# Kernel optimization log

Hardware: AMD Instinct MI355X
Metric: run time of the kernel (lower is better)

## Reference

```python
import jax, jax.numpy as jnp
import numpy as np

NX, NY = 128, 128
NT = 50
DECAY = 0.1
M1 = M2 = 12
WIDTH = 64


def _spectral(x, w1, w2):
    # x: [B, W, NX, NY]; w1/w2: complex [W, W, M1, M2]
    xf = jnp.fft.rfft2(x)                                   # [B, W, NX, NY//2+1]
    of = jnp.zeros(xf.shape[:2] + (NX, NY // 2 + 1), jnp.complex64)
    of = of.at[:, :, :M1, :M2].set(jnp.einsum('bixy,ioxy->boxy', xf[:, :, :M1, :M2], w1))
    of = of.at[:, :, NX - M1:, :M2].set(jnp.einsum('bixy,ioxy->boxy', xf[:, :, NX - M1:, :M2], w2))
    return jnp.fft.irfft2(of, s=(NX, NY))


def _forward(xyt_q, obs_coords, obs_vals, x_grid, y_grid,
             fc0_w, fc0_b, spec_w1r, spec_w1i, spec_w2r, spec_w2i,
             pw_w, pw_b, fc1_w, fc1_b, fc2_w, fc2_b,
             nb_idx, sensor_iy, sensor_ix, Lx, Ly):
    B, K = nb_idx.shape
    # ---- gather obs, temporal-decay weight, scatter-add into sparse grid ----
    sensor_ids = nb_idx // NT                               # [B, K]
    t_nb = obs_coords[nb_idx, 2]                            # [B, K]
    w = jnp.exp(-DECAY * jnp.abs(t_nb - xyt_q[:, None, 2])) # [B, K]
    vals = obs_vals[nb_idx] * w                             # [B, K]
    lin = sensor_iy[sensor_ids] * NY + sensor_ix[sensor_ids]
    flat = (lin + jnp.arange(B)[:, None] * (NX * NY)).ravel()
    sparse = jnp.zeros(B * NX * NY, obs_vals.dtype).at[flat].add(vals.ravel())
    counts = jnp.zeros(B * NX * NY, obs_vals.dtype).at[flat].add(w.ravel())
    grid = jnp.where(counts > 0, sparse / jnp.maximum(counts, 1e-6), 0.0).reshape(B, NX, NY)
    # ---- FNO core ----
    inp = jnp.stack([grid,
                     jnp.broadcast_to(x_grid, (B, NX, NY)),
                     jnp.broadcast_to(y_grid, (B, NX, NY))], axis=1)  # [B, 3, NX, NY]
    x = jnp.einsum('bcxy,cw->bwxy', inp, fc0_w) + fc0_b[None, :, None, None]
    for i in range(4):
        y = (_spectral(x, spec_w1r[i] + 1j * spec_w1i[i], spec_w2r[i] + 1j * spec_w2i[i])
             + jnp.einsum('bcxy,oc->boxy', x, pw_w[i]) + pw_b[i][None, :, None, None])
        x = jax.nn.gelu(y, approximate=False) if i < 3 else y
    h = jax.nn.gelu(jnp.einsum('bwxy,wf->bxyf', x, fc1_w) + fc1_b, approximate=False)
    field = (jnp.einsum('bxyf,fo->bxyo', h, fc2_w) + fc2_b).transpose(0, 3, 1, 2)  # [B, 3, NX, NY]
    # ---- bilinear sample at query points ----
    x01 = jnp.clip(xyt_q[:, 0] / max(Lx, 1e-6), 0.0, 1.0)
    y01 = jnp.clip(xyt_q[:, 1] / max(Ly, 1e-6), 0.0, 1.0)
    gx = x01 * (NX - 1)
    gy = y01 * (NY - 1)
    x0 = jnp.floor(gx).astype(jnp.int32)
    y0 = jnp.floor(gy).astype(jnp.int32)
    x1 = jnp.minimum(x0 + 1, NX - 1)
    y1 = jnp.minimum(y0 + 1, NY - 1)
    wx = (gx - x0)[:, None]
    wy = (gy - y0)[:, None]
    b = jnp.arange(B)
    f00 = field[b, :, x0, y0]
    f10 = field[b, :, x1, y0]
    f01 = field[b, :, x0, y1]
    f11 = field[b, :, x1, y1]
    top = f00 * (1.0 - wx) + f10 * wx
    bot = f01 * (1.0 - wx) + f11 * wx
    return top * (1.0 - wy) + bot * wy                       # [B, 3]


def setup_inputs() -> dict:
    key = jax.random.key(0)
    ks = jax.random.split(key, 20)
    B, K, NOBS, NS = 64, 64, 50000, 1000
    scale = 1.0 / (WIDTH * WIDTH)
    inp = {
        'xyt_q': jax.random.uniform(ks[0], (B, 3), jnp.float32),
        'obs_coords': jax.random.uniform(ks[1], (NOBS, 3), jnp.float32),
        'obs_vals': jax.random.normal(ks[2], (NOBS,), jnp.float32),
        'x_grid': jax.random.uniform(ks[3], (NX, NY), jnp.float32),
        'y_grid': jax.random.uniform(ks[4], (NX, NY), jnp.float32),
        'fc0_w': jax.random.normal(ks[5], (3, WIDTH), jnp.float32) * 0.3,
        'fc0_b': jnp.zeros((WIDTH,), jnp.float32),
        'spec_w1r': scale * jax.random.uniform(ks[6], (4, WIDTH, WIDTH, M1, M2), jnp.float32),
        'spec_w1i': scale * jax.random.uniform(ks[7], (4, WIDTH, WIDTH, M1, M2), jnp.float32),
        'spec_w2r': scale * jax.random.uniform(ks[8], (4, WIDTH, WIDTH, M1, M2), jnp.float32),
        'spec_w2i': scale * jax.random.uniform(ks[9], (4, WIDTH, WIDTH, M1, M2), jnp.float32),
        'pw_w': jax.random.normal(ks[10], (4, WIDTH, WIDTH), jnp.float32) * (1.0 / np.sqrt(WIDTH)),
        'pw_b': jnp.zeros((4, WIDTH), jnp.float32),
        'fc1_w': jax.random.normal(ks[11], (WIDTH, 128), jnp.float32) * (1.0 / np.sqrt(WIDTH)),
        'fc1_b': jnp.zeros((128,), jnp.float32),
        'fc2_w': jax.random.normal(ks[12], (128, 3), jnp.float32) * (1.0 / np.sqrt(128.0)),
        'fc2_b': jnp.zeros((3,), jnp.float32),
        'nb_idx': jax.random.randint(ks[13], (B, K), 0, NOBS, jnp.int32),
        'sensor_iy': jax.random.randint(ks[14], (NS,), 0, NX, jnp.int32),
        'sensor_ix': jax.random.randint(ks[15], (NS,), 0, NY, jnp.int32),
        'Lx': 1,
        'Ly': 1,
    }
    return inp


def reference(xyt_q, obs_coords, obs_vals, x_grid, y_grid,
              fc0_w, fc0_b, spec_w1r, spec_w1i, spec_w2r, spec_w2i,
              pw_w, pw_b, fc1_w, fc1_b, fc2_w, fc2_b,
              nb_idx, sensor_iy, sensor_ix, Lx, Ly):
    return _forward(xyt_q, obs_coords, obs_vals, x_grid, y_grid,
                    fc0_w, fc0_b, spec_w1r, spec_w1i, spec_w2r, spec_w2i,
                    pw_w, pw_b, fc1_w, fc1_b, fc2_w, fc2_b,
                    nb_idx, sensor_iy, sensor_ix, Lx, Ly)
```

## Files before the change

kernel.cpp:

```cpp
#include <hip/hip_runtime.h>
#include <math.h>

#define NXg 128
#define NYg 128
#define Pg  (NXg*NYg)
#define Bq  64
#define Wd  64
#define NKX 24
#define NMODE (NKX*12)
#define PI2_128 0.04908738521234052f

typedef _Float16 f16x8 __attribute__((ext_vector_type(8)));
typedef _Float16 f16x4 __attribute__((ext_vector_type(4)));
typedef float    f32x4 __attribute__((ext_vector_type(4)));

#define OFF_TC  0
#define OFF_TS  (OFF_TC + 128)
#define F32_END (OFF_TS + 128)
#define H_T1E  0
#define H_T1ET (H_T1E + 32*128)
#define H_A2   (H_T1ET + 128*32)
#define H_PWH  (H_A2 + 48*256)
#define H_T2ET (H_PWH + 4*64*64)
#define H_XFHR (H_T2ET + 128*64)
#define H_XFHI (H_XFHR + 288*4096)
#define H_OFHR (H_XFHI + 288*4096)
#define H_OFHI (H_OFHR + 288*4096)
#define H_WHR  (H_OFHI + 288*4096)
#define H_WHI  (H_WHR + (size_t)4*288*4096)
#define H_YG   (H_WHI + (size_t)4*288*4096)
#define H_X    (H_YG + (size_t)Bq*Wd*128*24)
#define H_U    (H_X + (size_t)Bq*128*128*64)

__device__ __forceinline__ float fast_gelu(float v) {
    float a = fabsf(v) * 0.70710678118654752f;
    float t = 1.f / (1.f + 0.3275911f * a);
    float p = t * (0.254829592f + t * (-0.284496736f + t * (1.421413741f +
              t * (-1.453152027f + t * 1.061405429f))));
    float er = 1.f - p * __expf(-a * a);
    er = copysignf(er, v);
    return 0.5f * v * (1.f + er);
}

__global__ void k_prep(_Float16* T1e_g, _Float16* T1eT_g, _Float16* A2_g,
                       const float* pww, _Float16* PWh, _Float16* T2eT_g,
                       float* Tc, float* Ts,
                       const float* xyt, const float* obs_c, const float* obs_v,
                       const int* nb, const int* siy, const int* six,
                       float* val, float* cnt,
                       const float* w1r, const float* w1i,
                       const float* w2r, const float* w2i,
                       _Float16* Whr, _Float16* Whi) {
    __shared__ _Float16 L[64][146];
    int blk = blockIdx.x;
    if (blk < 64) {
        int t = blk * 256 + threadIdx.x;
        if (t < 32*128) {
            int r = t >> 7, y = t & 127;
            float v = 0.f;
            if (r < 12)      v =  cosf((float)((r * y) & 127) * PI2_128);
            else if (r < 24) v = -sinf((float)(((r-12) * y) & 127) * PI2_128);
            T1e_g[t] = (_Float16)v;
            int y2 = t >> 5, r2 = t & 31;
            float v2 = 0.f;
            if (r2 < 12)      v2 =  cosf((float)((r2 * y2) & 127) * PI2_128);
            else if (r2 < 24) v2 = -sinf((float)(((r2-12) * y2) & 127) * PI2_128);
            T1eT_g[t] = (_Float16)v2;
        }
        if (t < 48*256) {
            int m = t >> 8, k = t & 255;
            int x = k & 127;
            int hi = (k >= 128);
            float v;
            if (m < 24) {
                int kx = (m < 12) ? m : (104 + m);
                float th = (float)((kx * x) & 127) * PI2_128;
                v = hi ? sinf(th) : cosf(th);
            } else {
                int mm = m - 24;
                int kx = (mm < 12) ? mm : (104 + mm);
                float th = (float)((kx * x) & 127) * PI2_128;
                v = hi ? cosf(th) : -sinf(th);
            }
            A2_g[t] = (_Float16)v;
        }
        if (t < 4*64*64) PWh[t] = (_Float16)pww[t];
        if (t < 128*64) {
            int x = t >> 6, k = t & 63;
            float v = 0.f;
            if (k < 24) {
                int kx = (k < 12) ? k : (104 + k);
                v = cosf((float)((kx * x) & 127) * PI2_128);
            } else if (k < 48) {
                int kk = k - 24;
                int kx = (kk < 12) ? kk : (104 + kk);
                v = sinf((float)((kx * x) & 127) * PI2_128);
            }
            T2eT_g[t] = (_Float16)v;
        }
        if (t < 128) {
            float th = (float)t * PI2_128;
            Tc[t] = cosf(th);
            Ts[t] = sinf(th);
        }
    } else if (blk < 80) {
        int t = (blk - 64) * 256 + threadIdx.x;
        int b = t >> 6;
        int id = nb[t];
        int sid = id / 50;
        float tq = xyt[b*3 + 2];
        float w = expf(-0.1f * fabsf(obs_c[id*3 + 2] - tq));
        int lin = siy[sid] * NYg + six[sid];
        atomicAdd(&val[b*Pg + lin], obs_v[id] * w);
        atomicAdd(&cnt[b*Pg + lin], w);
    } else {
        int u = blk - 80;
        int layer = u >> 8;
        int rem = u & 255;
        int o = rem & 63, ri = (rem >> 6) & 1, half = rem >> 7;
        const float* src = half ? (ri ? w2i : w2r) : (ri ? w1i : w1r);
        _Float16* dst = ri ? Whi : Whr;
        size_t sbase = (size_t)layer * 589824 + (size_t)o * 144;
        for (int idx = threadIdx.x; idx < 9216; idx += 256) {
            int i = idx / 144, m = idx - i*144;
            L[i][m] = (_Float16)src[sbase + (size_t)i*9216 + m];
        }
        __syncthreads();
        size_t obase = ((size_t)(layer*288 + half*144) << 12) + o*64;
        for (int idx = threadIdx.x; idx < 9216; idx += 256) {
            int m = idx >> 6, i = idx & 63;
            dst[obase + ((size_t)m << 12) + i] = L[i][m];
        }
    }
}

__device__ __forceinline__ void stageA_bf(const _Float16* __restrict__ T1e_g, int lane, f16x8* bf) {
    int l15 = lane & 15, quad = lane >> 4;
    #pragma unroll
    for (int u = 0; u < 8; u++) {
        int nt2 = u >> 2, q = u & 3;
        bf[u] = *(const f16x8*)&T1e_g[(nt2*16 + l15)*128 + q*32 + quad*8];
    }
}

__device__ __forceinline__ void stageA_core(const _Float16 (*Xn)[76], const f16x8* bf,
                                            _Float16* __restrict__ Yg, int b, int row, int tid) {
    int wave = tid >> 6, lane = tid & 63;
    int l15 = lane & 15, quad = lane >> 4;
    f16x8 af[4];
    #pragma unroll
    for (int q = 0; q < 4; q++)
        #pragma unroll
        for (int j = 0; j < 8; j++)
            af[q][j] = Xn[q*32 + quad*8 + j][wave*16 + l15];
    #pragma unroll
    for (int nt2 = 0; nt2 < 2; nt2++) {
        f32x4 acc = {0.f,0.f,0.f,0.f};
        #pragma unroll
        for (int q = 0; q < 4; q++)
            acc = __builtin_amdgcn_mfma_f32_16x16x32_f16(af[q], bf[nt2*4 + q], acc, 0, 0, 0);
        int t = nt2*16 + l15;
        if (t < 24) {
            #pragma unroll
            for (int r = 0; r < 4; r++) {
                int o = wave*16 + quad*4 + r;
                Yg[((size_t)(b*64 + o)*128 + row)*24 + t] = (_Float16)acc[r];
            }
        }
    }
}

__device__ __forceinline__ void stageA(const _Float16 (*Xn)[76], const _Float16* __restrict__ T1e_g,
                                       _Float16* __restrict__ Yg, int b, int row, int tid) {
    f16x8 bf[8];
    stageA_bf(T1e_g, tid & 63, bf);
    stageA_core(Xn, bf, Yg, b, row, tid);
}

__global__ __launch_bounds__(256) void k_fc0y(const float* __restrict__ val, const float* __restrict__ cnt,
                      const float* __restrict__ xg, const float* __restrict__ yg,
                      const float* __restrict__ w, const float* __restrict__ bb,
                      const _Float16* __restrict__ T1e_g,
                      _Float16* __restrict__ Yg) {
    __shared__ _Float16 Xn[128][76];
    __shared__ float wl[4][64];
    int row = blockIdx.x, b = blockIdx.y;
    int tid = threadIdx.x;
    if (tid < 64) {
        wl[0][tid] = w[tid]; wl[1][tid] = w[64+tid]; wl[2][tid] = w[128+tid]; wl[3][tid] = bb[tid];
    }
    __syncthreads();
    {
        int y = tid & 127, half = tid >> 7;
        int p = row*128 + y;
        float c = cnt[(size_t)b*Pg + p];
        float g = (c > 0.f) ? val[(size_t)b*Pg + p] / fmaxf(c, 1e-6f) : 0.f;
        float a1 = xg[p], a2 = yg[p];
        #pragma unroll
        for (int blk = 0; blk < 4; blk++) {
            f16x8 pk;
            #pragma unroll
            for (int j = 0; j < 8; j++) {
                int o = half*32 + blk*8 + j;
                pk[j] = (_Float16)(g*wl[0][o] + a1*wl[1][o] + a2*wl[2][o] + wl[3][o]);
            }
            *(f16x8*)&Xn[y][half*32 + blk*8] = pk;
        }
    }
    __syncthreads();
    stageA(Xn, T1e_g, Yg, b, row, tid);
}

__global__ __launch_bounds__(256) void k_sB(const _Float16* __restrict__ Yg,
                    const _Float16* __restrict__ A2_g,
                    _Float16* __restrict__ xfhr, _Float16* __restrict__ xfhi) {
    __shared__ _Float16 Ys[4][28][136];
    int bc4 = blockIdx.x << 2;
    int tid = threadIdx.x;
    int wave = tid >> 6, lane = tid & 63;
    int l15 = lane & 15, quad = lane >> 4;
    const _Float16* base = Yg + (size_t)bc4 * 3072;
    for (int i = tid; i < 1536; i += 256) {
        int s = i / 384, ii = i - s*384;
        f16x8 v = *(const f16x8*)&base[s*3072 + ii*8];
        int e = ii*8;
        #pragma unroll
        for (int j = 0; j < 8; j++) {
            int idx = e + j;
            int x = idx / 24, t = idx - x*24;
            Ys[s][t][x] = v[j];
        }
    }
    __syncthreads();
    int bc = bc4 + wave;
    #pragma unroll
    for (int mt = 0; mt < 3; mt++) {
        f32x4 acc = {0.f,0.f,0.f,0.f};
        #pragma unroll
        for (int q = 0; q < 8; q++) {
            f16x8 a = *(const f16x8*)&A2_g[(size_t)(mt*16 + l15)*256 + q*32 + quad*8];
            const _Float16* brow = (q < 4) ? &Ys[wave][l15][q*32 + quad*8]
                                           : &Ys[wave][12 + l15][(q-4)*32 + quad*8];
            f16x8 bfr = *(const f16x8*)brow;
            acc = __builtin_amdgcn_mfma_f32_16x16x32_f16(a, bfr, acc, 0, 0, 0);
        }
        if (l15 < 12) {
            #pragma unroll
            for (int r = 0; r < 4; r++) {
                int m = mt*16 + quad*4 + r;
                if (m < 24) xfhr[(size_t)(m*12 + l15)*4096 + bc] = (_Float16)acc[r];
                else        xfhi[(size_t)((m-24)*12 + l15)*4096 + bc] = (_Float16)acc[r];
            }
        }
    }
}

__global__ __launch_bounds__(256) void k_s3m(const _Float16* __restrict__ xfhr, const _Float16* __restrict__ xfhi,
                    const _Float16* __restrict__ Whr, const _Float16* __restrict__ Whi,
                    _Float16* __restrict__ ofhr, _Float16* __restrict__ ofhi, int layer) {
    __shared__ _Float16 Xr[16][72], Xi[16][72];
    int mode = blockIdx.x;
    int bo = blockIdx.y << 4;
    int tid = threadIdx.x;
    int wave = tid >> 6, lane = tid & 63;
    int l15 = lane & 15, quad = lane >> 4;
    const _Float16* pr = xfhr + (size_t)mode * 4096 + bo*64;
    const _Float16* pi = xfhi + (size_t)mode * 4096 + bo*64;
    if (tid < 128) {
        int b = tid >> 3, seg = tid & 7;
        *(f16x8*)&Xr[b][seg*8] = *(const f16x8*)&pr[tid*8];
        *(f16x8*)&Xi[b][seg*8] = *(const f16x8*)&pi[tid*8];
    }
    __syncthreads();
    size_t wb = ((size_t)(layer*288 + mode)*64 + wave*16 + l15) * 64 + quad*8;
    f16x8 wr0 = *(const f16x8*)&Whr[wb];
    f16x8 wr1 = *(const f16x8*)&Whr[wb + 32];
    f16x8 wi0 = *(const f16x8*)&Whi[wb];
    f16x8 wi1 = *(const f16x8*)&Whi[wb + 32];
    f16x8 xr0 = *(const f16x8*)&Xr[l15][quad*8];
    f16x8 xr1 = *(const f16x8*)&Xr[l15][32 + quad*8];
    f16x8 xi0 = *(const f16x8*)&Xi[l15][quad*8];
    f16x8 xi1 = *(const f16x8*)&Xi[l15][32 + quad*8];
    f16x8 xn0, xn1;
    #pragma unroll
    for (int j = 0; j < 8; j++) { xn0[j] = -xi0[j]; xn1[j] = -xi1[j]; }
    f32x4 cr = {0.f,0.f,0.f,0.f}, ci = {0.f,0.f,0.f,0.f};
    cr = __builtin_amdgcn_mfma_f32_16x16x32_f16(xr0, wr0, cr, 0, 0, 0);
    cr = __builtin_amdgcn_mfma_f32_16x16x32_f16(xr1, wr1, cr, 0, 0, 0);
    cr = __builtin_amdgcn_mfma_f32_16x16x32_f16(xn0, wi0, cr, 0, 0, 0);
    cr = __builtin_amdgcn_mfma_f32_16x16x32_f16(xn1, wi1, cr, 0, 0, 0);
    ci = __builtin_amdgcn_mfma_f32_16x16x32_f16(xr0, wi0, ci, 0, 0, 0);
    ci = __builtin_amdgcn_mfma_f32_16x16x32_f16(xr1, wi1, ci, 0, 0, 0);
    ci = __builtin_amdgcn_mfma_f32_16x16x32_f16(xi0, wr0, ci, 0, 0, 0);
    ci = __builtin_amdgcn_mfma_f32_16x16x32_f16(xi1, wr1, ci, 0, 0, 0);
    #pragma unroll
    for (int r = 0; r < 4; r++) {
        int b = bo + quad*4 + r;
        int o = wave*16 + l15;
        ofhr[(size_t)mode*4096 + b*64 + o] = (_Float16)cr[r];
        ofhi[(size_t)mode*4096 + b*64 + o] = (_Float16)ci[r];
    }
}

__global__ __launch_bounds__(256) void k_sG(const _Float16* __restrict__ ofhr, const _Float16* __restrict__ ofhi,
                    const _Float16* __restrict__ T2eT_g, _Float16* __restrict__ Gh) {
    __shared__ _Float16 As[64][72];
    __shared__ _Float16 Cs[128][72];
    int b = blockIdx.x, t = blockIdx.y;
    int tid = threadIdx.x;
    int wave = tid >> 6, lane = tid & 63;
    int l15 = lane & 15, quad = lane >> 4;
    int ky = (t < 12) ? t : (t - 12);
    float sc = ((ky == 0) ? 1.f : 2.f) * (1.f/16384.f);
    bool isReal = (t < 12);
    if (tid < 192) {
        int kxi = tid >> 3, seg = tid & 7;
        size_t idx = (size_t)(kxi*12 + ky)*4096 + b*64 + seg*8;
        f16x8 vr8 = *(const f16x8*)&ofhr[idx];
        f16x8 vi8 = *(const f16x8*)&ofhi[idx];
        #pragma unroll
        for (int j = 0; j < 8; j++) {
            int o = seg*8 + j;
            float vr = (float)vr8[j] * sc, vi = (float)vi8[j] * sc;
            As[o][kxi]      = (_Float16)(isReal ? vr : vi);
            As[o][24 + kxi] = (_Float16)(isReal ? -vi : vr);
        }
    }
    for (int i = tid; i < 1024; i += 256)
        As[i >> 4][48 + (i & 15)] = (_Float16)0.f;
    __syncthreads();
    f16x8 a0 = *(const f16x8*)&As[wave*16 + l15][quad*8];
    f16x8 a1 = *(const f16x8*)&As[wave*16 + l15][32 + quad*8];
    #pragma unroll
    for (int nt = 0; nt < 8; nt++) {
        f16x8 b0 = *(const f16x8*)&T2eT_g[(nt*16 + l15)*64 + quad*8];
        f16x8 b1 = *(const f16x8*)&T2eT_g[(nt*16 + l15)*64 + 32 + quad*8];
        f32x4 acc = {0.f,0.f,0.f,0.f};
        acc = __builtin_amdgcn_mfma_f32_16x16x32_f16(a0, b0, acc, 0, 0, 0);
        acc = __builtin_amdgcn_mfma_f32_16x16x32_f16(a1, b1, acc, 0, 0, 0);
        f16x4 pk;
        #pragma unroll
        for (int r = 0; r < 4; r++) pk[r] = (_Float16)acc[r];
        *(f16x4*)&Cs[nt*16 + l15][wave*16 + quad*4] = pk;
    }
    __syncthreads();
    float4* o4 = (float4*)Gh;
    for (int i = tid; i < 1024; i += 256) {
        int x = i >> 3, seg = i & 7;
        o4[((size_t)((b*128 + x)*24 + t))*8 + seg] = *(const float4*)&Cs[x][seg*8];
    }
}

__global__ __launch_bounds__(256, 4) void k_s45(_Float16* __restrict__ xh,
                    const _Float16* __restrict__ Gh,
                    const _Float16* __restrict__ T1e_g, const _Float16* __restrict__ T1eT_g,
                    const _Float16* __restrict__ PWh,
                    const float* __restrict__ pwb,
                    _Float16* __restrict__ Yg, int layer,
                    const float* __restrict__ xyt, const int* __restrict__ Lx,
                    const float* __restrict__ val, const float* __restrict__ cnt,
                    const float* __restrict__ xg, const float* __restrict__ yg,
                    const float* __restrict__ fc0w, const float* __restrict__ fc0b) {
    __shared__ _Float16 BsT[2][128][76];
    __shared__ float wl[4][64];
    int rp = blockIdx.x, b = blockIdx.y;
    int row0 = rp << 1;
    int tid = threadIdx.x;
    int wave = tid >> 6, lane = tid & 63;
    int l15 = lane & 15, quad = lane >> 4;

    f16x8 af2[2];
    #pragma unroll
    for (int r2 = 0; r2 < 2; r2++)
        #pragma unroll
        for (int j = 0; j < 8; j++) af2[r2][j] = (_Float16)0.f;
    if (quad < 3) {
        #pragma unroll
        for (int r2 = 0; r2 < 2; r2++) {
            const _Float16* gt = Gh + (size_t)(b*128 + row0 + r2) * 1536 + wave*16 + l15;
            #pragma unroll
            for (int j = 0; j < 8; j++) af2[r2][j] = gt[(quad*8 + j) * 64];
        }
    }

    f16x8 af0 = *(const f16x8*)&PWh[(size_t)(layer*64 + wave*16 + l15)*64 + quad*8];
    f16x8 af1 = *(const f16x8*)&PWh[(size_t)(layer*64 + wave*16 + l15)*64 + 32 + quad*8];
    f16x8 b2a[8];
    #pragma unroll
    for (int nt = 0; nt < 8; nt++)
        b2a[nt] = *(const f16x8*)&T1eT_g[(nt*16 + l15)*32 + quad*8];
    float pb[4];
    #pragma unroll
    for (int r = 0; r < 4; r++)
        pb[r] = pwb[layer*64 + wave*16 + quad*4 + r];

    if (layer == 0) {
        if (tid < 64) {
            wl[0][tid] = fc0w[tid]; wl[1][tid] = fc0w[64+tid];
            wl[2][tid] = fc0w[128+tid]; wl[3][tid] = fc0b[tid];
        }
        __syncthreads();
        int y = tid & 127, half = tid >> 7;
        #pragma unroll
        for (int r2 = 0; r2 < 2; r2++) {
            int p = (row0 + r2)*128 + y;
            float c = cnt[(size_t)b*Pg + p];
            float g = (c > 0.f) ? val[(size_t)b*Pg + p] / fmaxf(c, 1e-6f) : 0.f;
            float a1 = xg[p], a2 = yg[p];
            #pragma unroll
            for (int blk = 0; blk < 4; blk++) {
                f16x8 pkk;
                #pragma unroll
                for (int j = 0; j < 8; j++) {
                    int o = half*32 + blk*8 + j;
                    pkk[j] = (_Float16)(g*wl[0][o] + a1*wl[1][o] + a2*wl[2][o] + wl[3][o]);
                }
                *(f16x8*)&BsT[r2][y][half*32 + blk*8] = pkk;
            }
        }
    } else {
        for (int i = tid; i < 2048; i += 256) {
            int r2 = i >> 10, k = i & 1023;
            int y = k >> 3, seg = k & 7;
            *(float4*)&BsT[r2][y][seg*8] =
                ((const float4*)(xh + (size_t)(b*128 + row0 + r2) * 8192))[k];
        }
    }
    __syncthreads();

    f16x4 pk[2][8];
    #pragma unroll
    for (int r2 = 0; r2 < 2; r2++) {
        f32x4 acc[8];
        #pragma unroll
        for (int nt = 0; nt < 8; nt++) {
            f32x4 a = {0.f,0.f,0.f,0.f};
            f16x8 b0 = *(const f16x8*)&BsT[r2][nt*16 + l15][quad*8];
            f16x8 b1 = *(const f16x8*)&BsT[r2][nt*16 + l15][32 + quad*8];
            a = __builtin_amdgcn_mfma_f32_16x16x32_f16(af0, b0, a, 0, 0, 0);
            a = __builtin_amdgcn_mfma_f32_16x16x32_f16(af1, b1, a, 0, 0, 0);
            a = __builtin_amdgcn_mfma_f32_16x16x32_f16(af2[r2], b2a[nt], a, 0, 0, 0);
            acc[nt] = a;
        }
        #pragma unroll
        for (int nt = 0; nt < 8; nt++)
            #pragma unroll
            for (int r = 0; r < 4; r++)
                pk[r2][nt][r] = (_Float16)fast_gelu(acc[nt][r] + pb[r]);
    }
    __syncthreads();

    #pragma unroll
    for (int r2 = 0; r2 < 2; r2++)
        #pragma unroll
        for (int nt = 0; nt < 8; nt++)
            *(f16x4*)&BsT[r2][nt*16 + l15][wave*16 + quad*4] = pk[r2][nt];
    __syncthreads();

    bool st0 = true, st1 = true;
    if (layer == 2) {
        float Lxf = fmaxf((float)Lx[0], 1e-6f);
        float x01 = fminf(fmaxf(xyt[b*3 + 0] / Lxf, 0.f), 1.f);
        float gxp = x01 * (NXg - 1);
        int x0 = (int)floorf(gxp);
        int x1 = min(x0 + 1, NXg - 1);
        st0 = (row0 == x0) || (row0 == x1);
        st1 = (row0 + 1 == x0) || (row0 + 1 == x1);
    }
    for (int i = tid; i < 2048; i += 256) {
        int r2 = i >> 10, k = i & 1023;
        if (r2 ? st1 : st0) {
            int y = k >> 3, seg = k & 7;
            ((float4*)(xh + (size_t)(b*128 + row0 + r2) * 8192))[k] =
                *(const float4*)&BsT[r2][y][seg*8];
        }
    }

    f16x8 bf[8];
    stageA_bf(T1e_g, lane, bf);
    stageA_core(BsT[0], bf, Yg, b, row0, tid);
    stageA_core(BsT[1], bf, Yg, b, row0 + 1, tid);
}

__global__ __launch_bounds__(256) void k_final(const _Float16* __restrict__ x,
                    const _Float16* __restrict__ ofhr, const _Float16* __restrict__ ofhi,
                    const float* __restrict__ pw, const float* __restrict__ pwb,
                    const float* __restrict__ fc1w, const float* __restrict__ fc1b,
                    const float* __restrict__ fc2w, const float* __restrict__ fc2b,
                    const float* __restrict__ xyt, const int* __restrict__ Lx, const int* __restrict__ Ly,
                    const float* __restrict__ Tc, const float* __restrict__ Ts,
                    float* __restrict__ out) {
    __shared__ float y4[4][64];
    __shared__ float hh[4][129];
    __shared__ int   pxy[4][2];
    __shared__ float wxy[2];
    __shared__ float tc[128], ts[128];
    int b = blockIdx.x;
    if (threadIdx.x < 128) {
        tc[threadIdx.x] = Tc[threadIdx.x];
        ts[threadIdx.x] = Ts[threadIdx.x];
    }
    if (threadIdx.x == 0) {
        float Lxf = fmaxf((float)Lx[0], 1e-6f);
        float Lyf = fmaxf((float)Ly[0], 1e-6f);
        float x01 = fminf(fmaxf(xyt[b*3 + 0] / Lxf, 0.f), 1.f);
        float y01 = fminf(fmaxf(xyt[b*3 + 1] / Lyf, 0.f), 1.f);
        float gx = x01 * (NXg - 1), gy = y01 * (NYg - 1);
        int x0 = (int)floorf(gx), y0 = (int)floorf(gy);
        int x1 = min(x0 + 1, NXg - 1), y1 = min(y0 + 1, NYg - 1);
        wxy[0] = gx - (float)x0;
        wxy[1] = gy - (float)y0;
        pxy[0][0] = x0; pxy[0][1] = y0;
        pxy[1][0] = x1; pxy[1][1] = y0;
        pxy[2][0] = x0; pxy[2][1] = y1;
        pxy[3][0] = x1; pxy[3][1] = y1;
    }
    __syncthreads();
    {
        int p = threadIdx.x >> 6, o = threadIdx.x & 63;
        int px = pxy[p][0], py = pxy[p][1];
        float gkr[12], gki[12];
        #pragma unroll
        for (int ky = 0; ky < 12; ky++) { gkr[ky] = 0.f; gki[ky] = 0.f; }
        for (int kxi = 0; kxi < 24; kxi++) {
            int kx = (kxi < 12) ? kxi : (104 + kxi);
            int m = (kx * px) & 127;
            float cc = tc[m], ss = ts[m];
            #pragma unroll
            for (int ky = 0; ky < 12; ky++) {
                size_t idx = (size_t)(kxi*12 + ky)*4096 + b*64 + o;
                float a = (float)ofhr[idx], bb = (float)ofhi[idx];
                gkr[ky] += a*cc - bb*ss;
                gki[ky] += a*ss + bb*cc;
            }
        }
        float sp = gkr[0];
        #pragma unroll
        for (int ky = 1; ky < 12; ky++) {
            int m = (ky * py) & 127;
            sp += 2.f * (gkr[ky]*tc[m] - gki[ky]*ts[m]);
        }
        float s = 0.f;
        const _Float16* xb = x + ((size_t)(b*128 + px)*128 + py)*64;
        #pragma unroll 4
        for (int c = 0; c < 64; c++)
            s += pw[3*4096 + o*64 + c] * (float)xb[c];
        y4[p][o] = sp * (1.f/16384.f) + s + pwb[3*64 + o];
    }
    __syncthreads();
    for (int i = threadIdx.x; i < 512; i += 256) {
        int p = i >> 7, f = i & 127;
        float s = fc1b[f];
        #pragma unroll 4
        for (int w = 0; w < 64; w++) s += y4[p][w] * fc1w[w*128 + f];
        hh[p][f] = 0.5f * s * (1.f + erff(s * 0.70710678118654752f));
    }
    __syncthreads();
    if (threadIdx.x < 3) {
        int o3 = threadIdx.x;
        float f4[4];
        #pragma unroll
        for (int p = 0; p < 4; p++) {
            float s = fc2b[o3];
            #pragma unroll 4
            for (int f = 0; f < 128; f++) s += hh[p][f] * fc2w[f*3 + o3];
            f4[p] = s;
        }
        float wx = wxy[0], wy = wxy[1];
        float top = f4[0]*(1.f - wx) + f4[1]*wx;
        float bot = f4[2]*(1.f - wx) + f4[3]*wx;
        out[b*3 + o3] = top*(1.f - wy) + bot*wy;
    }
}

extern "C" void kernel_launch(void* const* d_in, const int* in_sizes, int n_in,
                              void* d_out, int out_size, void* d_ws, size_t ws_size,
                              hipStream_t stream) {
    const float* xyt    = (const float*)d_in[0];
    const float* obs_c  = (const float*)d_in[1];
    const float* obs_v  = (const float*)d_in[2];
    const float* xg     = (const float*)d_in[3];
    const float* yg     = (const float*)d_in[4];
    const float* fc0w   = (const float*)d_in[5];
    const float* fc0b   = (const float*)d_in[6];
    const float* w1r    = (const float*)d_in[7];
    const float* w1i    = (const float*)d_in[8];
    const float* w2r    = (const float*)d_in[9];
    const float* w2i    = (const float*)d_in[10];
    const float* pww    = (const float*)d_in[11];
    const float* pwb    = (const float*)d_in[12];
    const float* fc1w   = (const float*)d_in[13];
    const float* fc1b   = (const float*)d_in[14];
    const float* fc2w   = (const float*)d_in[15];
    const float* fc2b   = (const float*)d_in[16];
    const int*   nb     = (const int*)d_in[17];
    const int*   siy    = (const int*)d_in[18];
    const int*   six    = (const int*)d_in[19];
    const int*   Lx     = (const int*)d_in[20];
    const int*   Ly     = (const int*)d_in[21];
    float* out = (float*)d_out;

    float* W = (float*)d_ws;
    float* Tc  = W + OFF_TC;
    float* Ts  = W + OFF_TS;
    _Float16* Hbase = (_Float16*)(W + F32_END);
    _Float16* T1e_g  = Hbase + H_T1E;
    _Float16* T1eT_g = Hbase + H_T1ET;
    _Float16* A2_g   = Hbase + H_A2;
    _Float16* PWh    = Hbase + H_PWH;
    _Float16* T2eT_g = Hbase + H_T2ET;
    _Float16* xfhr   = Hbase + H_XFHR;
    _Float16* xfhi   = Hbase + H_XFHI;
    _Float16* ofhr   = Hbase + H_OFHR;
    _Float16* ofhi   = Hbase + H_OFHI;
    _Float16* Whr    = Hbase + H_WHR;
    _Float16* Whi    = Hbase + H_WHI;
    _Float16* Yg     = Hbase + H_YG;
    _Float16* xh     = Hbase + H_X;
    float*    val    = (float*)(Hbase + H_U);
    float*    cnt    = val + Bq*Pg;
    _Float16* Gh2    = Hbase + H_U + (size_t)4*Bq*Pg;

    hipMemsetAsync(val, 0, (size_t)2 * Bq * Pg * sizeof(float), stream);

    k_prep<<<1104, 256, 0, stream>>>(T1e_g, T1eT_g, A2_g, pww, PWh, T2eT_g, Tc, Ts,
                                     xyt, obs_c, obs_v, nb, siy, six, val, cnt,
                                     w1r, w1i, w2r, w2i, Whr, Whi);
    k_fc0y<<<dim3(128, Bq), 256, 0, stream>>>(val, cnt, xg, yg, fc0w, fc0b, T1e_g, Yg);

    for (int l = 0; l < 3; l++) {
        k_sB<<<Bq*Wd/4, 256, 0, stream>>>(Yg, A2_g, xfhr, xfhi);
        k_s3m<<<dim3(288, 4), 256, 0, stream>>>(xfhr, xfhi, Whr, Whi, ofhr, ofhi, l);
        k_sG<<<dim3(Bq, 24), 256, 0, stream>>>(ofhr, ofhi, T2eT_g, Gh2);
        k_s45<<<dim3(64, Bq), 256, 0, stream>>>(xh, Gh2, T1e_g, T1eT_g, PWh, pwb, Yg, l,
                                                xyt, Lx, val, cnt, xg, yg, fc0w, fc0b);
    }
    k_sB<<<Bq*Wd/4, 256, 0, stream>>>(Yg, A2_g, xfhr, xfhi);
    k_s3m<<<dim3(288, 4), 256, 0, stream>>>(xfhr, xfhi, Whr, Whi, ofhr, ofhi, 3);
    k_final<<<Bq, 256, 0, stream>>>(xh, ofhr, ofhi, pww, pwb, fc1w, fc1b, fc2w, fc2b,
                                    xyt, Lx, Ly, Tc, Ts, out);
}
```

Before: 615.7 us.

## Stage stage-A outputs in LDS and store Yg row-contiguous with coalesced writes

Stage-A MFMA results used to be written straight to global memory as scattered 2-byte stores in a [b][o][row][t] layout. They are now staged in shared memory, reusing the input tile after an extra barrier, and written out as contiguous float4 stores in a [b][row][o][t] layout. The consumer kernel k_sB is changed to read this new layout, gathering each x row across strided global locations. The cost is extra barriers and a less contiguous read pattern in k_sB, in exchange for coalesced writes in the producers.

After: 618.6 us. About the same (+0.5%).

```diff
diff --git a/kernel.cpp b/kernel.cpp
--- a/kernel.cpp
+++ b/kernel.cpp
@@ -143,16 +143,20 @@
     }
 }
 
-__device__ __forceinline__ void stageA_core(const _Float16 (*Xn)[76], const f16x8* bf,
-                                            _Float16* __restrict__ Yg, int b, int row, int tid) {
+__device__ __forceinline__ void stageA_af(const _Float16 (*Xn)[76], int tid, f16x8* af) {
     int wave = tid >> 6, lane = tid & 63;
     int l15 = lane & 15, quad = lane >> 4;
-    f16x8 af[4];
     #pragma unroll
     for (int q = 0; q < 4; q++)
         #pragma unroll
         for (int j = 0; j < 8; j++)
             af[q][j] = Xn[q*32 + quad*8 + j][wave*16 + l15];
+}
+
+__device__ __forceinline__ void stageA_lds(const f16x8* af, const f16x8* bf,
+                                           _Float16* Yl, int tid) {
+    int wave = tid >> 6, lane = tid & 63;
+    int l15 = lane & 15, quad = lane >> 4;
     #pragma unroll
     for (int nt2 = 0; nt2 < 2; nt2++) {
         f32x4 acc = {0.f,0.f,0.f,0.f};
@@ -162,19 +166,10 @@
         int t = nt2*16 + l15;
         if (t < 24) {
             #pragma unroll
-            for (int r = 0; r < 4; r++) {
-                int o = wave*16 + quad*4 + r;
-                Yg[((size_t)(b*64 + o)*128 + row)*24 + t] = (_Float16)acc[r];
-            }
-        }
-    }
-}
-
-__device__ __forceinline__ void stageA(const _Float16 (*Xn)[76], const _Float16* __restrict__ T1e_g,
-                                       _Float16* __restrict__ Yg, int b, int row, int tid) {
-    f16x8 bf[8];
-    stageA_bf(T1e_g, tid & 63, bf);
-    stageA_core(Xn, bf, Yg, b, row, tid);
+            for (int r = 0; r < 4; r++)
+                Yl[(wave*16 + quad*4 + r)*24 + t] = (_Float16)acc[r];
+        }
+    }
 }
 
 __global__ __launch_bounds__(256) void k_fc0y(const float* __restrict__ val, const float* __restrict__ cnt,
@@ -208,7 +203,16 @@
         }
     }
     __syncthreads();
-    stageA(Xn, T1e_g, Yg, b, row, tid);
+    f16x8 bf[8];
+    stageA_bf(T1e_g, tid & 63, bf);
+    f16x8 af[4];
+    stageA_af(Xn, tid, af);
+    __syncthreads();
+    _Float16* Yl = &Xn[0][0];
+    stageA_lds(af, bf, Yl, tid);
+    __syncthreads();
+    if (tid < 192)
+        ((float4*)(Yg + (size_t)(b*128 + row) * 1536))[tid] = ((const float4*)Yl)[tid];
 }
 
 __global__ __launch_bounds__(256) void k_sB(const _Float16* __restrict__ Yg,
@@ -219,15 +223,16 @@
     int tid = threadIdx.x;
     int wave = tid >> 6, lane = tid & 63;
     int l15 = lane & 15, quad = lane >> 4;
-    const _Float16* base = Yg + (size_t)bc4 * 3072;
+    int b = bc4 >> 6, c0 = bc4 & 63;
+    const _Float16* base = Yg + ((size_t)b*128*64 + c0)*24;
     for (int i = tid; i < 1536; i += 256) {
-        int s = i / 384, ii = i - s*384;
-        f16x8 v = *(const f16x8*)&base[s*3072 + ii*8];
-        int e = ii*8;
+        int x = i / 12, w = i - x*12;
+        f16x8 v = *(const f16x8*)&base[(size_t)x*1536 + w*8];
+        int e = w*8;
         #pragma unroll
         for (int j = 0; j < 8; j++) {
-            int idx = e + j;
-            int x = idx / 24, t = idx - x*24;
+            int tt = e + j;
+            int s = tt / 24, t = tt - s*24;
             Ys[s][t][x] = v[j];
         }
     }
@@ -478,8 +483,20 @@
 
     f16x8 bf[8];
     stageA_bf(T1e_g, lane, bf);
-    stageA_core(BsT[0], bf, Yg, b, row0, tid);
-    stageA_core(BsT[1], bf, Yg, b, row0 + 1, tid);
+    f16x8 afA[4], afB[4];
+    stageA_af(BsT[0], tid, afA);
+    stageA_af(BsT[1], tid, afB);
+    __syncthreads();
+    _Float16* Yl = &BsT[0][0][0];
+    stageA_lds(afA, bf, Yl, tid);
+    stageA_lds(afB, bf, Yl + 1536, tid);
+    __syncthreads();
+    for (int i = tid; i < 384; i += 256) {
+        int r2 = i >= 192;
+        int j = i - r2*192;
+        ((float4*)(Yg + (size_t)(b*128 + row0 + r2) * 1536))[j] =
+            ((const float4*)(Yl + r2*1536))[j];
+    }
 }
 
 __global__ __launch_bounds__(256) void k_final(const _Float16* __restrict__ x,
```
